# Performance work log

Hardware: AMD Instinct MI355X
Metric: run time of the kernel (lower is better)

## Reference

```python
import jax, jax.numpy as jnp
import numpy as np

TOPK = 8
ROUTE_SCALE = 2.5


def setup_inputs() -> dict:
    key = jax.random.key(0)
    k1, k2 = jax.random.split(key)
    N, D, E = 16384, 2048, 64
    x = jax.random.normal(k1, (N, D), dtype=jnp.float32)
    # kaiming_uniform-ish scale for the router weight
    bound = 1.0 / np.sqrt(D)
    weight = jax.random.uniform(k2, (E, D), dtype=jnp.float32, minval=-bound, maxval=bound)
    expert_bias = jnp.zeros((E,), dtype=jnp.float32)
    return {"x": x, "weight": weight, "expert_bias": expert_bias}


def reference(x, weight, expert_bias):
    # linear scorer: (N, D) @ (D, E) -> (N, E)
    scores = jax.nn.sigmoid(jnp.einsum('nd,ed->ne', x.astype(jnp.float32), weight.astype(jnp.float32)))
    original_scores = scores
    # aux-loss-free routing: add dynamic per-expert bias for selection only
    routing_scores = scores + expert_bias[None, :]
    _, indices = jax.lax.top_k(routing_scores, TOPK)          # (N, TOPK) int32
    weights = jnp.take_along_axis(original_scores, indices, axis=1)  # gather original (un-biased) scores
    # sigmoid scoring -> renormalize the selected weights
    weights = weights / (jnp.sum(weights, axis=-1, keepdims=True) + 1e-8)
    weights = weights * ROUTE_SCALE
    return weights.astype(x.dtype), indices
```

## Files before the change

### kernel.cpp

```cpp
#include <hip/hip_runtime.h>
#include <math.h>


#define D_DIM 2048
#define E_DIM 64
#define TOPK 8
#define TM 32
#define BK 64
#define XS 68
#define WS 68
#define SCS 65

__global__ __launch_bounds__(256) void expert_gate_kernel(
    const float* __restrict__ x,
    const float* __restrict__ w,
    const float* __restrict__ bias,
    float* __restrict__ out,
    int N)
{
    __shared__ float Xs[TM * XS];
    __shared__ float Ws[E_DIM * WS];
    __shared__ float Sc[TM * SCS];

    const int t    = threadIdx.x;
    const int tx   = t & 15;
    const int ty   = t >> 4;
    const int tok0 = blockIdx.x * TM;
    const int lane = t & 63;
    const float my_bias = bias[lane];

    float c[2][4][4];
    #pragma unroll
    for (int i = 0; i < 2; ++i)
        #pragma unroll
        for (int e = 0; e < 4; ++e)
            #pragma unroll
            for (int l = 0; l < 4; ++l) c[i][e][l] = 0.f;

    for (int k0 = 0; k0 < D_DIM; k0 += BK) {
        {
            int f = t;
            int row = f >> 4, col = (f & 15) << 2;
            float4 v = *reinterpret_cast<const float4*>(
                &x[(size_t)(tok0 + row) * D_DIM + k0 + col]);
            *reinterpret_cast<float4*>(&Xs[row * XS + col]) = v;
            f = t + 256;
            row = f >> 4; col = (f & 15) << 2;
            v = *reinterpret_cast<const float4*>(
                &x[(size_t)(tok0 + row) * D_DIM + k0 + col]);
            *reinterpret_cast<float4*>(&Xs[row * XS + col]) = v;
        }
        #pragma unroll
        for (int i = 0; i < 4; ++i) {
            int f = t + i * 256;
            int row = f >> 4, col = (f & 15) << 2;
            float4 v = *reinterpret_cast<const float4*>(
                &w[(size_t)row * D_DIM + k0 + col]);
            *reinterpret_cast<float4*>(&Ws[row * WS + col]) = v;
        }
        __syncthreads();

        #pragma unroll
        for (int g = 0; g < 4; ++g) {
            float4 xa[2][4];
            #pragma unroll
            for (int i = 0; i < 2; ++i)
                #pragma unroll
                for (int j = 0; j < 4; ++j)
                    xa[i][j] = *reinterpret_cast<const float4*>(
                        &Xs[(ty + 16 * i) * XS + g * 16 + 4 * j]);
            float4 wb[4][4];
            #pragma unroll
            for (int e = 0; e < 4; ++e)
                #pragma unroll
                for (int j = 0; j < 4; ++j)
                    wb[e][j] = *reinterpret_cast<const float4*>(
                        &Ws[(tx + 16 * e) * WS + g * 16 + 4 * j]);

            #pragma unroll
            for (int j = 3; j >= 0; --j) {
                #pragma unroll
                for (int i = 0; i < 2; ++i) {
                    #pragma unroll
                    for (int e = 0; e < 4; ++e) {
                        c[i][e][0] = __fadd_rn(c[i][e][0], __fmul_rn(xa[i][j].x, wb[e][j].x));
                        c[i][e][1] = __fadd_rn(c[i][e][1], __fmul_rn(xa[i][j].y, wb[e][j].y));
                        c[i][e][2] = __fadd_rn(c[i][e][2], __fmul_rn(xa[i][j].z, wb[e][j].z));
                        c[i][e][3] = __fadd_rn(c[i][e][3], __fmul_rn(xa[i][j].w, wb[e][j].w));
                    }
                }
            }
        }
        __syncthreads();
    }

    #pragma unroll
    for (int i = 0; i < 2; ++i) {
        #pragma unroll
        for (int e = 0; e < 4; ++e) {
            float z = __fadd_rn(__fadd_rn(c[i][e][0], c[i][e][1]),
                                __fadd_rn(c[i][e][2], c[i][e][3]));
            float ez = (float)exp(-(double)z);
            float s  = __fdiv_rn(1.0f, __fadd_rn(1.0f, ez));
            Sc[(ty + 16 * i) * SCS + (tx + 16 * e)] = s;
        }
    }
    __syncthreads();

    const int wave = t >> 6;
    for (int r = 0; r < 8; ++r) {
        const int tok = wave * 8 + r;
        const float s = Sc[tok * SCS + lane];
        float rv = __fadd_rn(s, my_bias);
        float outw = 0.f;
        int   outi = 0;
        float ssum = 0.f;
        #pragma unroll
        for (int sel = 0; sel < TOPK; ++sel) {
            float v = rv;
            int   vi = lane;
            #pragma unroll
            for (int off = 1; off < 64; off <<= 1) {
                float ov = __shfl_xor(v, off);
                int   oi = __shfl_xor(vi, off);
                if (ov > v || (ov == v && oi < vi)) { v = ov; vi = oi; }
            }
            float cs = __shfl(s, vi);
            ssum = __fadd_rn(ssum, cs);
            if (lane == sel) { outw = cs; outi = vi; }
            if (lane == vi) rv = -INFINITY;
        }
        if (lane < TOPK) {
            const size_t base = (size_t)(tok0 + tok) * TOPK + lane;
            out[base] = __fmul_rn(__fdiv_rn(outw, __fadd_rn(ssum, 1e-8f)), 2.5f);
            out[(size_t)N * TOPK + base] = (float)outi;
        }
    }
}

extern "C" void kernel_launch(void* const* d_in, const int* in_sizes, int n_in,
                              void* d_out, int out_size, void* d_ws, size_t ws_size,
                              hipStream_t stream) {
    const float* x    = (const float*)d_in[0];
    const float* w    = (const float*)d_in[1];
    const float* bias = (const float*)d_in[2];
    float* out = (float*)d_out;
    const int N = in_sizes[0] / D_DIM;
    const int grid = N / TM;
    expert_gate_kernel<<<grid, 256, 0, stream>>>(x, w, bias, out, N);
}
```

Before: 290.4 us.

## Double-buffer shared memory tiles with register prefetch of next K slice

The K loop now uses two shared-memory buffers for the X and W tiles. The next slice is loaded from global memory into registers before the current slice's FMAs and stored into the alternate buffer afterwards, so global latency overlaps compute and one barrier per iteration is removed. The cost is double the X/W shared memory (about 52KB total per block) and extra registers for the staged float4s, which may reduce occupancy.

```diff
diff --git a/kernel.cpp b/kernel.cpp
--- a/kernel.cpp
+++ b/kernel.cpp
@@ -7,9 +7,12 @@
 #define TOPK 8
 #define TM 32
 #define BK 64
+#define NR (D_DIM / BK)
 #define XS 68
 #define WS 68
 #define SCS 65
+#define XHALF (TM * XS)
+#define WHALF (E_DIM * WS)
 
 __global__ __launch_bounds__(256) void expert_gate_kernel(
     const float* __restrict__ x,
@@ -18,8 +21,8 @@
     float* __restrict__ out,
     int N)
 {
-    __shared__ float Xs[TM * XS];
-    __shared__ float Ws[E_DIM * WS];
+    __shared__ float Xs[2 * XHALF];
+    __shared__ float Ws[2 * WHALF];
     __shared__ float Sc[TM * SCS];
 
     const int t    = threadIdx.x;
@@ -29,6 +32,15 @@
     const int lane = t & 63;
     const float my_bias = bias[lane];
 
+    const int srow = t >> 4;
+    const int scol = (t & 15) << 2;
+    const float* xp0 = &x[(size_t)(tok0 + srow) * D_DIM + scol];
+    const float* xp1 = &x[(size_t)(tok0 + 16 + srow) * D_DIM + scol];
+    const float* wp  = &w[(size_t)srow * D_DIM + scol];
+    const int xw0 = srow * XS + scol;
+    const int xw1 = (srow + 16) * XS + scol;
+    const int ww0 = srow * WS + scol;
+
     float c[2][4][4];
     #pragma unroll
     for (int i = 0; i < 2; ++i)
@@ -37,28 +49,35 @@
             #pragma unroll
             for (int l = 0; l < 4; ++l) c[i][e][l] = 0.f;
 
-    for (int k0 = 0; k0 < D_DIM; k0 += BK) {
-        {
-            int f = t;
-            int row = f >> 4, col = (f & 15) << 2;
-            float4 v = *reinterpret_cast<const float4*>(
-                &x[(size_t)(tok0 + row) * D_DIM + k0 + col]);
-            *reinterpret_cast<float4*>(&Xs[row * XS + col]) = v;
-            f = t + 256;
-            row = f >> 4; col = (f & 15) << 2;
-            v = *reinterpret_cast<const float4*>(
-                &x[(size_t)(tok0 + row) * D_DIM + k0 + col]);
-            *reinterpret_cast<float4*>(&Xs[row * XS + col]) = v;
+    float4 sx0 = *reinterpret_cast<const float4*>(xp0);
+    float4 sx1 = *reinterpret_cast<const float4*>(xp1);
+    float4 sw0 = *reinterpret_cast<const float4*>(wp);
+    float4 sw1 = *reinterpret_cast<const float4*>(wp + 16 * D_DIM);
+    float4 sw2 = *reinterpret_cast<const float4*>(wp + 32 * D_DIM);
+    float4 sw3 = *reinterpret_cast<const float4*>(wp + 48 * D_DIM);
+    xp0 += BK; xp1 += BK; wp += BK;
+    *reinterpret_cast<float4*>(&Xs[xw0]) = sx0;
+    *reinterpret_cast<float4*>(&Xs[xw1]) = sx1;
+    *reinterpret_cast<float4*>(&Ws[ww0]) = sw0;
+    *reinterpret_cast<float4*>(&Ws[ww0 + 16 * WS]) = sw1;
+    *reinterpret_cast<float4*>(&Ws[ww0 + 32 * WS]) = sw2;
+    *reinterpret_cast<float4*>(&Ws[ww0 + 48 * WS]) = sw3;
+    __syncthreads();
+
+    for (int s = 0; s < NR; ++s) {
+        const int cur = s & 1;
+        const float* Xc = Xs + cur * XHALF;
+        const float* Wc = Ws + cur * WHALF;
+
+        if (s + 1 < NR) {
+            sx0 = *reinterpret_cast<const float4*>(xp0);
+            sx1 = *reinterpret_cast<const float4*>(xp1);
+            sw0 = *reinterpret_cast<const float4*>(wp);
+            sw1 = *reinterpret_cast<const float4*>(wp + 16 * D_DIM);
+            sw2 = *reinterpret_cast<const float4*>(wp + 32 * D_DIM);
+            sw3 = *reinterpret_cast<const float4*>(wp + 48 * D_DIM);
+            xp0 += BK; xp1 += BK; wp += BK;
         }
-        #pragma unroll
-        for (int i = 0; i < 4; ++i) {
-            int f = t + i * 256;
-            int row = f >> 4, col = (f & 15) << 2;
-            float4 v = *reinterpret_cast<const float4*>(
-                &w[(size_t)row * D_DIM + k0 + col]);
-            *reinterpret_cast<float4*>(&Ws[row * WS + col]) = v;
-        }
-        __syncthreads();
 
         #pragma unroll
         for (int g = 0; g < 4; ++g) {
@@ -68,14 +87,14 @@
                 #pragma unroll
                 for (int j = 0; j < 4; ++j)
                     xa[i][j] = *reinterpret_cast<const float4*>(
-                        &Xs[(ty + 16 * i) * XS + g * 16 + 4 * j]);
+                        &Xc[(ty + 16 * i) * XS + g * 16 + 4 * j]);
             float4 wb[4][4];
             #pragma unroll
             for (int e = 0; e < 4; ++e)
                 #pragma unroll
                 for (int j = 0; j < 4; ++j)
                     wb[e][j] = *reinterpret_cast<const float4*>(
-                        &Ws[(tx + 16 * e) * WS + g * 16 + 4 * j]);
+                        &Wc[(tx + 16 * e) * WS + g * 16 + 4 * j]);
 
             #pragma unroll
             for (int j = 3; j >= 0; --j) {
@@ -91,6 +110,17 @@
                 }
             }
         }
+
+        if (s + 1 < NR) {
+            float* Xn = Xs + (cur ^ 1) * XHALF;
+            float* Wn = Ws + (cur ^ 1) * WHALF;
+            *reinterpret_cast<float4*>(&Xn[xw0]) = sx0;
+            *reinterpret_cast<float4*>(&Xn[xw1]) = sx1;
+            *reinterpret_cast<float4*>(&Wn[ww0]) = sw0;
+            *reinterpret_cast<float4*>(&Wn[ww0 + 16 * WS]) = sw1;
+            *reinterpret_cast<float4*>(&Wn[ww0 + 32 * WS]) = sw2;
+            *reinterpret_cast<float4*>(&Wn[ww0 + 48 * WS]) = sw3;
+        }
         __syncthreads();
     }
 
@@ -101,8 +131,8 @@
             float z = __fadd_rn(__fadd_rn(c[i][e][0], c[i][e][1]),
                                 __fadd_rn(c[i][e][2], c[i][e][3]));
             float ez = (float)exp(-(double)z);
-            float s  = __fdiv_rn(1.0f, __fadd_rn(1.0f, ez));
-            Sc[(ty + 16 * i) * SCS + (tx + 16 * e)] = s;
+            float sg = __fdiv_rn(1.0f, __fadd_rn(1.0f, ez));
+            Sc[(ty + 16 * i) * SCS + (tx + 16 * e)] = sg;
         }
     }
     __syncthreads();
@@ -110,8 +140,8 @@
     const int wave = t >> 6;
     for (int r = 0; r < 8; ++r) {
         const int tok = wave * 8 + r;
-        const float s = Sc[tok * SCS + lane];
-        float rv = __fadd_rn(s, my_bias);
+        const float sg = Sc[tok * SCS + lane];
+        float rv = __fadd_rn(sg, my_bias);
         float outw = 0.f;
         int   outi = 0;
         float ssum = 0.f;
@@ -125,7 +155,7 @@
                 int   oi = __shfl_xor(vi, off);
                 if (ov > v || (ov == v && oi < vi)) { v = ov; vi = oi; }
             }
-            float cs = __shfl(s, vi);
+            float cs = __shfl(sg, vi);
             ssum = __fadd_rn(ssum, cs);
             if (lane == sel) { outw = cs; outi = vi; }
             if (lane == vi) rv = -INFINITY;
```

New measurement: 423.6 us. +45.9%, slower.

## Halve token tile, use packed v2f math, and raise occupancy bounds

Applied to the files above, without the earlier changes.

Cuts the token tile from 32 to 16 so each thread holds 4x4 accumulators instead of 2x4x4, and adds a launch-bounds hint for 4 blocks per CU. The inner product now uses two-wide vector multiply-add, which can map to packed FP32 instructions, with fp contraction disabled so rounding stays separate. Load addresses are hoisted into pointers that advance each step. The grid doubles and each block reloads the full 64x2048 weight slice over half as many tokens, so weight traffic through L2 and LDS doubles relative to x.

```diff
diff --git a/kernel.cpp b/kernel.cpp
--- a/kernel.cpp
+++ b/kernel.cpp
@@ -2,22 +2,28 @@
 #include <math.h>
 
 
+#pragma clang fp contract(off)
+
 #define D_DIM 2048
 #define E_DIM 64
 #define TOPK 8
-#define TM 32
+#define TM 16
 #define BK 64
+#define NR (D_DIM / BK)
 #define XS 68
 #define WS 68
 #define SCS 65
 
-__global__ __launch_bounds__(256) void expert_gate_kernel(
+typedef float v2f __attribute__((ext_vector_type(2)));
+
+__global__ __launch_bounds__(256, 4) void expert_gate_kernel(
     const float* __restrict__ x,
     const float* __restrict__ w,
     const float* __restrict__ bias,
     float* __restrict__ out,
     int N)
 {
+#pragma clang fp contract(off)
     __shared__ float Xs[TM * XS];
     __shared__ float Ws[E_DIM * WS];
     __shared__ float Sc[TM * SCS];
@@ -29,46 +35,36 @@
     const int lane = t & 63;
     const float my_bias = bias[lane];
 
-    float c[2][4][4];
+    const int srow = t >> 4;
+    const int scol = (t & 15) << 2;
+    const float* xp = &x[(size_t)(tok0 + srow) * D_DIM + scol];
+    const float* wp = &w[(size_t)srow * D_DIM + scol];
+    const int xw = srow * XS + scol;
+    const int ww = srow * WS + scol;
+
+    v2f c01[4], c23[4];
     #pragma unroll
-    for (int i = 0; i < 2; ++i)
-        #pragma unroll
-        for (int e = 0; e < 4; ++e)
-            #pragma unroll
-            for (int l = 0; l < 4; ++l) c[i][e][l] = 0.f;
+    for (int e = 0; e < 4; ++e) { c01[e] = (v2f)(0.f); c23[e] = (v2f)(0.f); }
 
-    for (int k0 = 0; k0 < D_DIM; k0 += BK) {
-        {
-            int f = t;
-            int row = f >> 4, col = (f & 15) << 2;
-            float4 v = *reinterpret_cast<const float4*>(
-                &x[(size_t)(tok0 + row) * D_DIM + k0 + col]);
-            *reinterpret_cast<float4*>(&Xs[row * XS + col]) = v;
-            f = t + 256;
-            row = f >> 4; col = (f & 15) << 2;
-            v = *reinterpret_cast<const float4*>(
-                &x[(size_t)(tok0 + row) * D_DIM + k0 + col]);
-            *reinterpret_cast<float4*>(&Xs[row * XS + col]) = v;
-        }
+    for (int s = 0; s < NR; ++s) {
+        float4 v = *reinterpret_cast<const float4*>(xp);
+        xp += BK;
+        *reinterpret_cast<float4*>(&Xs[xw]) = v;
         #pragma unroll
         for (int i = 0; i < 4; ++i) {
-            int f = t + i * 256;
-            int row = f >> 4, col = (f & 15) << 2;
-            float4 v = *reinterpret_cast<const float4*>(
-                &w[(size_t)row * D_DIM + k0 + col]);
-            *reinterpret_cast<float4*>(&Ws[row * WS + col]) = v;
+            float4 u = *reinterpret_cast<const float4*>(wp + i * 16 * D_DIM);
+            *reinterpret_cast<float4*>(&Ws[ww + i * 16 * WS]) = u;
         }
+        wp += BK;
         __syncthreads();
 
         #pragma unroll
         for (int g = 0; g < 4; ++g) {
-            float4 xa[2][4];
+            float4 xa[4];
             #pragma unroll
-            for (int i = 0; i < 2; ++i)
-                #pragma unroll
-                for (int j = 0; j < 4; ++j)
-                    xa[i][j] = *reinterpret_cast<const float4*>(
-                        &Xs[(ty + 16 * i) * XS + g * 16 + 4 * j]);
+            for (int j = 0; j < 4; ++j)
+                xa[j] = *reinterpret_cast<const float4*>(
+                    &Xs[ty * XS + g * 16 + 4 * j]);
             float4 wb[4][4];
             #pragma unroll
             for (int e = 0; e < 4; ++e)
@@ -79,15 +75,14 @@
 
             #pragma unroll
             for (int j = 3; j >= 0; --j) {
+                const v2f xlo = *reinterpret_cast<const v2f*>(&xa[j].x);
+                const v2f xhi = *reinterpret_cast<const v2f*>(&xa[j].z);
                 #pragma unroll
-                for (int i = 0; i < 2; ++i) {
-                    #pragma unroll
-                    for (int e = 0; e < 4; ++e) {
-                        c[i][e][0] = __fadd_rn(c[i][e][0], __fmul_rn(xa[i][j].x, wb[e][j].x));
-                        c[i][e][1] = __fadd_rn(c[i][e][1], __fmul_rn(xa[i][j].y, wb[e][j].y));
-                        c[i][e][2] = __fadd_rn(c[i][e][2], __fmul_rn(xa[i][j].z, wb[e][j].z));
-                        c[i][e][3] = __fadd_rn(c[i][e][3], __fmul_rn(xa[i][j].w, wb[e][j].w));
-                    }
+                for (int e = 0; e < 4; ++e) {
+                    const v2f wlo = *reinterpret_cast<const v2f*>(&wb[e][j].x);
+                    const v2f whi = *reinterpret_cast<const v2f*>(&wb[e][j].z);
+                    c01[e] = c01[e] + xlo * wlo;
+                    c23[e] = c23[e] + xhi * whi;
                 }
             }
         }
@@ -95,37 +90,34 @@
     }
 
     #pragma unroll
-    for (int i = 0; i < 2; ++i) {
-        #pragma unroll
-        for (int e = 0; e < 4; ++e) {
-            float z = __fadd_rn(__fadd_rn(c[i][e][0], c[i][e][1]),
-                                __fadd_rn(c[i][e][2], c[i][e][3]));
-            float ez = (float)exp(-(double)z);
-            float s  = __fdiv_rn(1.0f, __fadd_rn(1.0f, ez));
-            Sc[(ty + 16 * i) * SCS + (tx + 16 * e)] = s;
-        }
+    for (int e = 0; e < 4; ++e) {
+        float z = __fadd_rn(__fadd_rn(c01[e].x, c01[e].y),
+                            __fadd_rn(c23[e].x, c23[e].y));
+        float ez = (float)exp(-(double)z);
+        float sg = __fdiv_rn(1.0f, __fadd_rn(1.0f, ez));
+        Sc[ty * SCS + (tx + 16 * e)] = sg;
     }
     __syncthreads();
 
     const int wave = t >> 6;
-    for (int r = 0; r < 8; ++r) {
-        const int tok = wave * 8 + r;
-        const float s = Sc[tok * SCS + lane];
-        float rv = __fadd_rn(s, my_bias);
+    for (int r = 0; r < 4; ++r) {
+        const int tok = wave * 4 + r;
+        const float sg = Sc[tok * SCS + lane];
+        float rv = __fadd_rn(sg, my_bias);
         float outw = 0.f;
         int   outi = 0;
         float ssum = 0.f;
         #pragma unroll
         for (int sel = 0; sel < TOPK; ++sel) {
-            float v = rv;
+            float vv = rv;
             int   vi = lane;
             #pragma unroll
             for (int off = 1; off < 64; off <<= 1) {
-                float ov = __shfl_xor(v, off);
+                float ov = __shfl_xor(vv, off);
                 int   oi = __shfl_xor(vi, off);
-                if (ov > v || (ov == v && oi < vi)) { v = ov; vi = oi; }
+                if (ov > vv || (ov == vv && oi < vi)) { vv = ov; vi = oi; }
             }
-            float cs = __shfl(s, vi);
+            float cs = __shfl(sg, vi);
             ssum = __fadd_rn(ssum, cs);
             if (lane == sel) { outw = cs; outi = vi; }
             if (lane == vi) rv = -INFINITY;
```

New measurement: 318.2 us. +9.6%, slower.
